# Kernel tuning notes

Measured on AMD Instinct MI355X. Metric: run time of the kernel, lower is better.

## Reference

```python
import jax, jax.numpy as jnp
import numpy as np

N_NODES = 50000
N_EDGES = 1600000
N_FEAT = 128
DIM = 128
N_GRAPHS = 128
BN_EPS = 1e-5


def setup_inputs() -> dict:
    key = jax.random.key(0)
    ks = jax.random.split(key, 16)
    x = jax.random.normal(ks[0], (N_NODES, N_FEAT), dtype=jnp.float32)
    edge_index = jax.random.randint(ks[1], (2, N_EDGES), 0, N_NODES)
    batch = jnp.sort(jax.random.randint(ks[2], (N_NODES,), 0, N_GRAPHS))
    def lin(k, fin, fout):
        return jax.random.normal(k, (fin, fout), dtype=jnp.float32) / np.sqrt(fin).astype(np.float32)
    inp = {"x": x, "edge_index": edge_index, "batch": batch}
    fins = [N_FEAT, DIM, DIM]
    for i in range(3):
        inp[f"W{i}"] = lin(ks[3 + i], fins[i], DIM)
        inp[f"b{i}"] = jnp.zeros((DIM,), jnp.float32)
        inp[f"g{i}"] = jnp.ones((DIM,), jnp.float32)
        inp[f"be{i}"] = jnp.zeros((DIM,), jnp.float32)
    return inp


def _gcn_norm(edge_index, n):
    # add self loops, symmetric normalization D^-1/2 (A+I) D^-1/2
    loop = jnp.arange(n, dtype=edge_index.dtype)
    src = jnp.concatenate([edge_index[0], loop])
    dst = jnp.concatenate([edge_index[1], loop])
    deg = jax.ops.segment_sum(jnp.ones_like(src, dtype=jnp.float32), dst, num_segments=n)
    dinv = jnp.where(deg > 0, jax.lax.rsqrt(deg), 0.0)
    norm = dinv[src] * dinv[dst]  # [E+N]
    return src, dst, norm


def _gcn_conv(h, W, b, src, dst, norm, n):
    h = h @ W                      # [N, D]
    msg = h[src] * norm[:, None]   # [E+N, D] gather + scale
    agg = jax.ops.segment_sum(msg, dst, num_segments=n)
    return agg + b


def _batchnorm(h, g, be):
    mu = jnp.mean(h, axis=0)
    var = jnp.mean(jnp.square(h - mu), axis=0)  # biased, training-mode BN
    return (h - mu) * jax.lax.rsqrt(var + BN_EPS) * g + be


def reference(x, edge_index, batch, W0, b0, g0, be0, W1, b1, g1, be1, W2, b2, g2, be2):
    n = x.shape[0]
    src, dst, norm = _gcn_norm(edge_index, n)
    params = [(W0, b0, g0, be0), (W1, b1, g1, be1), (W2, b2, g2, be2)]
    h = x
    pools = []
    for (W, b, g, be) in params:
        h = jax.nn.relu(_gcn_conv(h, W, b, src, dst, norm, n))
        h = _batchnorm(h, g, be)
        pools.append(jax.ops.segment_sum(h, batch, num_segments=N_GRAPHS))
    return jnp.concatenate(pools, axis=1)  # [N_GRAPHS, 3*DIM]
```

## Files before the change

kernel.cpp:

```cpp
#include <hip/hip_runtime.h>
#include <hip/hip_bf16.h>

#define N_GRAPHS 128
#define BN_EPS 1e-5f
#define CHUNK 8192
#define NBU 512
#define CAP 8192

typedef short bf16x8 __attribute__((ext_vector_type(8)));
typedef short s16x4 __attribute__((ext_vector_type(4)));
typedef float f32x4 __attribute__((ext_vector_type(4)));

__device__ __forceinline__ unsigned short f2b(float f) {
    unsigned int u = __builtin_bit_cast(unsigned int, f);
    u += 0x7FFFu + ((u >> 16) & 1u);
    return (unsigned short)(u >> 16);
}
__device__ __forceinline__ float b2f_lo(unsigned int p) {
    return __builtin_bit_cast(float, p << 16);
}
__device__ __forceinline__ float b2f_hi(unsigned int p) {
    return __builtin_bit_cast(float, p & 0xFFFF0000u);
}

__global__ __launch_bounds__(512) void bin_chunks(const int* __restrict__ src,
                                                  const int* __restrict__ dst,
                                                  unsigned int* __restrict__ bpairs,
                                                  int* __restrict__ cnts,
                                                  int* __restrict__ cbase, int E) {
    __shared__ int lhist[NBU], lscan[NBU], lfill[NBU];
    int tid = threadIdx.x;
    int c0 = blockIdx.x * CHUNK;
    int ecnt = min(CHUNK, E - c0);
    lhist[tid] = 0;
    __syncthreads();
    for (int i = tid; i < ecnt; i += 512)
        atomicAdd(&lhist[((unsigned)dst[c0 + i]) >> 7], 1);
    __syncthreads();
    int orig = lhist[tid];
    lscan[tid] = orig;
    __syncthreads();
    for (int off = 1; off < NBU; off <<= 1) {
        int t = (tid >= off) ? lscan[tid - off] : 0;
        __syncthreads();
        lscan[tid] += t;
        __syncthreads();
    }
    int excl = lscan[tid] - orig;
    cnts[blockIdx.x * NBU + tid] = orig;
    cbase[blockIdx.x * NBU + tid] = excl;
    lfill[tid] = 0;
    __syncthreads();
    lscan[tid] = excl;
    __syncthreads();
    for (int i = tid; i < ecnt; i += 512) {
        int d = dst[c0 + i], s = src[c0 + i];
        int b = ((unsigned)d) >> 7;
        int pos = lscan[b] + atomicAdd(&lfill[b], 1);
        bpairs[c0 + pos] = ((unsigned)(d & 127) << 25) | (unsigned)s;
    }
}

__global__ __launch_bounds__(512) void bucket_scan(const int* __restrict__ cnts,
                                                   int* __restrict__ bucket_base, int nchunks) {
    __shared__ int s[NBU];
    int b = threadIdx.x;
    int tot = 0;
    for (int c = 0; c < nchunks; ++c) tot += cnts[c * NBU + b];
    s[b] = tot;
    __syncthreads();
    for (int off = 1; off < NBU; off <<= 1) {
        int t = (b >= off) ? s[b - off] : 0;
        __syncthreads();
        s[b] += t;
        __syncthreads();
    }
    bucket_base[b] = s[b] - tot;
}

__global__ __launch_bounds__(256) void bucket_csr(const unsigned int* __restrict__ bpairs,
                                                  const int* __restrict__ cnts,
                                                  const int* __restrict__ cbase,
                                                  const int* __restrict__ bucket_base,
                                                  int* __restrict__ rowp,
                                                  int* __restrict__ degarr,
                                                  float* __restrict__ dinv,
                                                  int* __restrict__ csr,
                                                  int nchunks, int N) {
    __shared__ unsigned int lpr[CAP];
    __shared__ int lcsr[CAP];
    __shared__ int ccnt[256], cofs[256], cb[256];
    __shared__ int lhist[128], lofs[128], lfill[128];
    int tid = threadIdx.x;
    int b = blockIdx.x;
    int bb = bucket_base[b];
    int total = bucket_base[b + 1] - bb;
    if (total > CAP) total = CAP;

    ccnt[tid] = (tid < nchunks) ? cnts[tid * NBU + b] : 0;
    cb[tid]   = (tid < nchunks) ? cbase[tid * NBU + b] : 0;
    cofs[tid] = ccnt[tid];
    __syncthreads();
    int orig = cofs[tid];
    for (int off = 1; off < 256; off <<= 1) {
        int t = (tid >= off) ? cofs[tid - off] : 0;
        __syncthreads();
        cofs[tid] += t;
        __syncthreads();
    }
    int o = cofs[tid] - orig;
    if (tid < nchunks) {
        int len = ccnt[tid];
        const unsigned int* p = bpairs + (size_t)tid * CHUNK + cb[tid];
        for (int i = 0; i < len; ++i) {
            int q = o + i;
            if (q < CAP) lpr[q] = p[i];
        }
    }
    if (tid < 128) { lhist[tid] = 0; lfill[tid] = 0; }
    __syncthreads();
    for (int i = tid; i < total; i += 256)
        atomicAdd(&lhist[lpr[i] >> 25], 1);
    __syncthreads();
    if (tid < 128) lofs[tid] = lhist[tid];
    __syncthreads();
    for (int off = 1; off < 128; off <<= 1) {
        int t = 0;
        if (tid < 128 && tid >= off) t = lofs[tid - off];
        __syncthreads();
        if (tid < 128) lofs[tid] += t;
        __syncthreads();
    }
    if (tid < 128) {
        int v = b * 128 + tid;
        if (v < N) {
            int dg = lhist[tid];
            degarr[v] = dg;
            rowp[v] = bb + lofs[tid] - dg;
            dinv[v] = rsqrtf((float)(dg + 1));
        }
    }
    __syncthreads();
    for (int i = tid; i < total; i += 256) {
        unsigned int pr = lpr[i];
        int dl = pr >> 25;
        int pos = lofs[dl] - lhist[dl] + atomicAdd(&lfill[dl], 1);
        if (pos < CAP) lcsr[pos] = (int)(pr & 0x1FFFFFFu);
    }
    __syncthreads();
    for (int i = tid; i < total; i += 256) csr[bb + i] = lcsr[i];
}

template <int AF32>
__global__ __launch_bounds__(256) void gemm_mfma(const void* __restrict__ Avoid,
                                                 const float* __restrict__ W,
                                                 unsigned short* __restrict__ Cb, int N) {
    __shared__ unsigned short sWt[128 * 128];
    int tid = threadIdx.x;
    for (int i = tid; i < 128 * 128; i += 256) {
        int k = i >> 7, c = i & 127;
        int kk = k & 31, k0 = k >> 5;
        int hi = (kk >> 2) & 3;
        int e = (kk & 3) + 4 * (kk >> 4);
        int idx = c * 128 + k0 * 32 + hi * 8 + e;
        sWt[idx ^ ((c & 7) << 3)] = f2b(W[i]);
    }
    __syncthreads();

    int wave = tid >> 6, lane = tid & 63;
    int lo4 = lane & 15, hi = lane >> 4;
    int rowBase = blockIdx.x * 256 + wave * 64;

    f32x4 acc[8][4];
#pragma unroll
    for (int ct = 0; ct < 8; ++ct)
#pragma unroll
        for (int rt = 0; rt < 4; ++rt) acc[ct][rt] = (f32x4){0.f, 0.f, 0.f, 0.f};

    const float* Af = (const float*)Avoid;
    const unsigned short* Ab = (const unsigned short*)Avoid;

    for (int k0 = 0; k0 < 128; k0 += 32) {
        bf16x8 bfrag[4];
#pragma unroll
        for (int rt = 0; rt < 4; ++rt) {
            int r = rowBase + rt * 16 + lo4;
            if (r >= N) r = N - 1;
            if (AF32) {
                float4 f0 = *(const float4*)(Af + (size_t)r * 128 + k0 + 4 * hi);
                float4 f1 = *(const float4*)(Af + (size_t)r * 128 + k0 + 16 + 4 * hi);
                bf16x8 f;
                f[0] = (short)f2b(f0.x); f[1] = (short)f2b(f0.y);
                f[2] = (short)f2b(f0.z); f[3] = (short)f2b(f0.w);
                f[4] = (short)f2b(f1.x); f[5] = (short)f2b(f1.y);
                f[6] = (short)f2b(f1.z); f[7] = (short)f2b(f1.w);
                bfrag[rt] = f;
            } else {
                s16x4 a0 = *(const s16x4*)(Ab + (size_t)r * 128 + k0 + 4 * hi);
                s16x4 a1 = *(const s16x4*)(Ab + (size_t)r * 128 + k0 + 16 + 4 * hi);
                bf16x8 f;
                f[0] = a0[0]; f[1] = a0[1]; f[2] = a0[2]; f[3] = a0[3];
                f[4] = a1[0]; f[5] = a1[1]; f[6] = a1[2]; f[7] = a1[3];
                bfrag[rt] = f;
            }
        }
        int kq = k0 >> 5;
#pragma unroll
        for (int ct = 0; ct < 8; ++ct) {
            int c = ct * 16 + lo4;
            int idx = (c * 128 + kq * 32 + hi * 8) ^ ((c & 7) << 3);
            bf16x8 af = *(const bf16x8*)(sWt + idx);
#pragma unroll
            for (int rt = 0; rt < 4; ++rt)
                acc[ct][rt] = __builtin_amdgcn_mfma_f32_16x16x32_bf16(af, bfrag[rt], acc[ct][rt], 0, 0, 0);
        }
    }

#pragma unroll
    for (int rt = 0; rt < 4; ++rt) {
        int r = rowBase + rt * 16 + lo4;
        if (r < N) {
#pragma unroll
            for (int ct = 0; ct < 8; ++ct) {
                int c0 = ct * 16 + hi * 4;
                ushort4 s;
                s.x = f2b(acc[ct][rt][0]);
                s.y = f2b(acc[ct][rt][1]);
                s.z = f2b(acc[ct][rt][2]);
                s.w = f2b(acc[ct][rt][3]);
                *(ushort4*)(Cb + (size_t)r * 128 + c0) = s;
            }
        }
    }
}

__global__ __launch_bounds__(256) void agg_relu_b16(const unsigned int* __restrict__ hW32,
                                                    const int* __restrict__ rowp,
                                                    const int* __restrict__ cnt,
                                                    const int* __restrict__ csr,
                                                    const float* __restrict__ dinv,
                                                    const float* __restrict__ bias,
                                                    unsigned int* __restrict__ z32, int N) {
    int wave = threadIdx.x >> 6, lane = threadIdx.x & 63;
    int v = blockIdx.x * 4 + wave;
    if (v >= N) return;
    int beg = rowp[v];
    int num = cnt[v];
    float s0 = 0.f, s1 = 0.f;
    int i = 0;
    for (; i + 4 <= num; i += 4) {
        int u0 = csr[beg + i + 0];
        int u1 = csr[beg + i + 1];
        int u2 = csr[beg + i + 2];
        int u3 = csr[beg + i + 3];
        float w0 = dinv[u0], w1 = dinv[u1], w2 = dinv[u2], w3 = dinv[u3];
        unsigned int p0 = hW32[(size_t)u0 * 64 + lane];
        unsigned int p1 = hW32[(size_t)u1 * 64 + lane];
        unsigned int p2 = hW32[(size_t)u2 * 64 + lane];
        unsigned int p3 = hW32[(size_t)u3 * 64 + lane];
        s0 += w0 * b2f_lo(p0) + w1 * b2f_lo(p1) + w2 * b2f_lo(p2) + w3 * b2f_lo(p3);
        s1 += w0 * b2f_hi(p0) + w1 * b2f_hi(p1) + w2 * b2f_hi(p2) + w3 * b2f_hi(p3);
    }
    for (; i < num; ++i) {
        int u = csr[beg + i];
        float w = dinv[u];
        unsigned int p = hW32[(size_t)u * 64 + lane];
        s0 += w * b2f_lo(p);
        s1 += w * b2f_hi(p);
    }
    float dv = dinv[v];
    unsigned int pv = hW32[(size_t)v * 64 + lane];
    s0 = dv * s0 + dv * dv * b2f_lo(pv) + bias[2 * lane];
    s1 = dv * s1 + dv * dv * b2f_hi(pv) + bias[2 * lane + 1];
    unsigned int po = (unsigned int)f2b(fmaxf(s0, 0.f)) | ((unsigned int)f2b(fmaxf(s1, 0.f)) << 16);
    z32[(size_t)v * 64 + lane] = po;
}

__global__ __launch_bounds__(256) void bn_stats_b16(const unsigned int* __restrict__ z32,
                                                    float* __restrict__ stats, int N) {
    int lane = threadIdx.x & 63, sub = threadIdx.x >> 6;
    float s0 = 0.f, s1 = 0.f, q0 = 0.f, q1 = 0.f;
    for (int v = blockIdx.x * 4 + sub; v < N; v += gridDim.x * 4) {
        unsigned int p = z32[(size_t)v * 64 + lane];
        float a = b2f_lo(p), c = b2f_hi(p);
        s0 += a; q0 = fmaf(a, a, q0);
        s1 += c; q1 = fmaf(c, c, q1);
    }
    __shared__ float ls[256][4];
    ls[threadIdx.x][0] = s0; ls[threadIdx.x][1] = s1;
    ls[threadIdx.x][2] = q0; ls[threadIdx.x][3] = q1;
    __syncthreads();
    if (sub == 0) {
        for (int k = 1; k < 4; ++k) {
            s0 += ls[lane + 64 * k][0]; s1 += ls[lane + 64 * k][1];
            q0 += ls[lane + 64 * k][2]; q1 += ls[lane + 64 * k][3];
        }
        atomicAdd(&stats[2 * lane], s0);
        atomicAdd(&stats[2 * lane + 1], s1);
        atomicAdd(&stats[128 + 2 * lane], q0);
        atomicAdd(&stats[129 + 2 * lane], q1);
    }
}

__global__ void bn_finalize(const float* __restrict__ stats, const float* __restrict__ g,
                            const float* __restrict__ be, float* __restrict__ ss, float invN) {
    int d = threadIdx.x;
    float mu = stats[d] * invN;
    float var = stats[128 + d] * invN - mu * mu;
    float sc = g[d] * rsqrtf(var + BN_EPS);
    ss[d] = sc;
    ss[128 + d] = be[d] - mu * sc;
}

__global__ __launch_bounds__(64) void apply_pool_b16(const unsigned int* __restrict__ z32,
                                                     const float* __restrict__ ss,
                                                     const int* __restrict__ batch,
                                                     float* __restrict__ out,
                                                     unsigned int* __restrict__ zb,
                                                     int layer, int N) {
    __shared__ int gb[32];
    int lane = threadIdx.x;
    int v0 = blockIdx.x * 32;
    int vend = min(v0 + 32, N);
    int cntv = vend - v0;
    if (lane < cntv) gb[lane] = batch[v0 + lane];
    __syncthreads();
    float sc0 = ss[2 * lane], sc1 = ss[2 * lane + 1];
    float sh0 = ss[128 + 2 * lane], sh1 = ss[129 + 2 * lane];
    float a0 = 0.f, a1 = 0.f;
    int cur = gb[0];
    for (int j = 0; j < cntv; ++j) {
        unsigned int p = z32[(size_t)(v0 + j) * 64 + lane];
        float x0 = fmaf(b2f_lo(p), sc0, sh0);
        float x1 = fmaf(b2f_hi(p), sc1, sh1);
        if (zb) zb[(size_t)(v0 + j) * 64 + lane] =
            (unsigned int)f2b(x0) | ((unsigned int)f2b(x1) << 16);
        int g = gb[j];
        if (g != cur) {
            atomicAdd(&out[(size_t)cur * 384 + layer * 128 + 2 * lane], a0);
            atomicAdd(&out[(size_t)cur * 384 + layer * 128 + 2 * lane + 1], a1);
            a0 = a1 = 0.f;
            cur = g;
        }
        a0 += x0; a1 += x1;
    }
    atomicAdd(&out[(size_t)cur * 384 + layer * 128 + 2 * lane], a0);
    atomicAdd(&out[(size_t)cur * 384 + layer * 128 + 2 * lane + 1], a1);
}

extern "C" void kernel_launch(void* const* d_in, const int* in_sizes, int n_in,
                              void* d_out, int out_size, void* d_ws, size_t ws_size,
                              hipStream_t stream) {
    const float* x    = (const float*)d_in[0];
    const int* eidx   = (const int*)d_in[1];
    const int* batch  = (const int*)d_in[2];

    const int N = in_sizes[2];
    const int E = in_sizes[1] / 2;
    const int* src = eidx;
    const int* dst = eidx + E;

    const int nchunks = (E + CHUNK - 1) / CHUNK;
    const int NB = (N + 127) / 128;

    size_t off = 0;
    auto alloc = [&](size_t bytes) {
        void* p = (char*)d_ws + off;
        off += (bytes + 255) & ~(size_t)255;
        return p;
    };
    unsigned short* hWb = (unsigned short*)alloc((size_t)N * 128 * 2);
    unsigned int* zb    = (unsigned int*)alloc((size_t)N * 64 * 4);
    unsigned int* z32   = (unsigned int*)alloc((size_t)N * 64 * 4);
    unsigned int* bpairs= (unsigned int*)alloc((size_t)nchunks * CHUNK * 4);
    int*   csr   = (int*)alloc((size_t)E * 4);
    int*   cnts  = (int*)alloc((size_t)nchunks * NBU * 4);
    int*   cbase = (int*)alloc((size_t)nchunks * NBU * 4);
    int*   bbase = (int*)alloc((size_t)(NBU + 1) * 4);
    int*   degar = (int*)alloc((size_t)N * 4);
    int*   rowp  = (int*)alloc((size_t)N * 4);
    float* dinv  = (float*)alloc((size_t)N * 4);
    float* stats = (float*)alloc(3 * 256 * 4);
    float* ss    = (float*)alloc(3 * 256 * 4);

    float* out = (float*)d_out;

    hipMemsetAsync(stats, 0, 3 * 256 * 4, stream);
    hipMemsetAsync(out, 0, (size_t)N_GRAPHS * 384 * 4, stream);

    bin_chunks<<<nchunks, 512, 0, stream>>>(src, dst, bpairs, cnts, cbase, E);
    bucket_scan<<<1, 512, 0, stream>>>(cnts, bbase, nchunks);
    bucket_csr<<<NB, 256, 0, stream>>>(bpairs, cnts, cbase, bbase, rowp, degar, dinv, csr,
                                       nchunks, N);

    const int gemm_blocks = (N + 255) / 256;
    const int agg_blocks  = (N + 3) / 4;
    const int pool_blocks = (N + 31) / 32;

    for (int l = 0; l < 3; ++l) {
        const float* W  = (const float*)d_in[3 + 4 * l];
        const float* b  = (const float*)d_in[4 + 4 * l];
        const float* g  = (const float*)d_in[5 + 4 * l];
        const float* be = (const float*)d_in[6 + 4 * l];

        if (l == 0)
            gemm_mfma<1><<<gemm_blocks, 256, 0, stream>>>((const void*)x, W, hWb, N);
        else
            gemm_mfma<0><<<gemm_blocks, 256, 0, stream>>>((const void*)zb, W, hWb, N);

        agg_relu_b16<<<agg_blocks, 256, 0, stream>>>((const unsigned int*)hWb, rowp, degar, csr,
                                                     dinv, b, z32, N);
        bn_stats_b16<<<256, 256, 0, stream>>>(z32, stats + l * 256, N);
        bn_finalize<<<1, 128, 0, stream>>>(stats + l * 256, g, be, ss + l * 256, 1.0f / N);
        apply_pool_b16<<<pool_blocks, 64, 0, stream>>>(z32, ss + l * 256, batch, out,
                                                       (l < 2) ? zb : (unsigned int*)nullptr, l, N);
    }
}
```

Baseline: 525.2 us.

## Fold BN affine into next GEMM, slab-partition features for aggregation, atomic bucket totals

Folds the BatchNorm scale into the next layer's weights and the shift into a per-column bias computed in bn_finalize. This removes the normalized zb write in apply_pool, and the next GEMM reads z32 directly. The GEMM output becomes a 4-slab layout of 32 columns each, and aggregation runs one slab per block, with 4 lanes-groups over 16 dwords splitting neighbors and reducing by shuffles, so the gather working set per slab is smaller and more cache-friendly. Bucket totals are accumulated atomically in bin_chunks instead of serially summed in bucket_scan. The cost is 4x more aggregation blocks re-reading the CSR and dinv per slab, and bf16 rounding of the scaled weights.

```diff
diff --git a/kernel.cpp b/kernel.cpp
--- a/kernel.cpp
+++ b/kernel.cpp
@@ -27,7 +27,8 @@
                                                   const int* __restrict__ dst,
                                                   unsigned int* __restrict__ bpairs,
                                                   int* __restrict__ cnts,
-                                                  int* __restrict__ cbase, int E) {
+                                                  int* __restrict__ cbase,
+                                                  int* __restrict__ btot, int E) {
     __shared__ int lhist[NBU], lscan[NBU], lfill[NBU];
     int tid = threadIdx.x;
     int c0 = blockIdx.x * CHUNK;
@@ -38,6 +39,7 @@
         atomicAdd(&lhist[((unsigned)dst[c0 + i]) >> 7], 1);
     __syncthreads();
     int orig = lhist[tid];
+    atomicAdd(&btot[tid], orig);
     lscan[tid] = orig;
     __syncthreads();
     for (int off = 1; off < NBU; off <<= 1) {
@@ -61,12 +63,11 @@
     }
 }
 
-__global__ __launch_bounds__(512) void bucket_scan(const int* __restrict__ cnts,
-                                                   int* __restrict__ bucket_base, int nchunks) {
+__global__ __launch_bounds__(512) void bucket_scan(const int* __restrict__ btot,
+                                                   int* __restrict__ bucket_base) {
     __shared__ int s[NBU];
     int b = threadIdx.x;
-    int tot = 0;
-    for (int c = 0; c < nchunks; ++c) tot += cnts[c * NBU + b];
+    int tot = btot[b];
     s[b] = tot;
     __syncthreads();
     for (int off = 1; off < NBU; off <<= 1) {
@@ -154,16 +155,20 @@
 template <int AF32>
 __global__ __launch_bounds__(256) void gemm_mfma(const void* __restrict__ Avoid,
                                                  const float* __restrict__ W,
+                                                 const float* __restrict__ ssPrev,
+                                                 const float* __restrict__ wb,
                                                  unsigned short* __restrict__ Cb, int N) {
     __shared__ unsigned short sWt[128 * 128];
     int tid = threadIdx.x;
     for (int i = tid; i < 128 * 128; i += 256) {
         int k = i >> 7, c = i & 127;
+        float w = W[i];
+        if (!AF32) w *= ssPrev[k];
         int kk = k & 31, k0 = k >> 5;
         int hi = (kk >> 2) & 3;
         int e = (kk & 3) + 4 * (kk >> 4);
         int idx = c * 128 + k0 * 32 + hi * 8 + e;
-        sWt[idx ^ ((c & 7) << 3)] = f2b(W[i]);
+        sWt[idx ^ ((c & 7) << 3)] = f2b(w);
     }
     __syncthreads();
 
@@ -223,57 +228,62 @@
 #pragma unroll
             for (int ct = 0; ct < 8; ++ct) {
                 int c0 = ct * 16 + hi * 4;
+                float4 wbv = make_float4(0.f, 0.f, 0.f, 0.f);
+                if (!AF32) wbv = *(const float4*)(wb + c0);
                 ushort4 s;
-                s.x = f2b(acc[ct][rt][0]);
-                s.y = f2b(acc[ct][rt][1]);
-                s.z = f2b(acc[ct][rt][2]);
-                s.w = f2b(acc[ct][rt][3]);
-                *(ushort4*)(Cb + (size_t)r * 128 + c0) = s;
+                s.x = f2b(acc[ct][rt][0] + wbv.x);
+                s.y = f2b(acc[ct][rt][1] + wbv.y);
+                s.z = f2b(acc[ct][rt][2] + wbv.z);
+                s.w = f2b(acc[ct][rt][3] + wbv.w);
+                int q = c0 >> 5;
+                *(ushort4*)(Cb + (size_t)q * N * 32 + (size_t)r * 32 + (c0 & 31)) = s;
             }
         }
     }
 }
 
-__global__ __launch_bounds__(256) void agg_relu_b16(const unsigned int* __restrict__ hW32,
-                                                    const int* __restrict__ rowp,
-                                                    const int* __restrict__ cnt,
-                                                    const int* __restrict__ csr,
-                                                    const float* __restrict__ dinv,
-                                                    const float* __restrict__ bias,
-                                                    unsigned int* __restrict__ z32, int N) {
+__global__ __launch_bounds__(256) void agg_relu_slab(const unsigned int* __restrict__ hW32,
+                                                     const int* __restrict__ rowp,
+                                                     const int* __restrict__ cnt,
+                                                     const int* __restrict__ csr,
+                                                     const float* __restrict__ dinv,
+                                                     const float* __restrict__ bias,
+                                                     unsigned int* __restrict__ z32,
+                                                     int ngroups, int N) {
+    int q = blockIdx.x / ngroups;
+    int group = blockIdx.x % ngroups;
     int wave = threadIdx.x >> 6, lane = threadIdx.x & 63;
-    int v = blockIdx.x * 4 + wave;
+    int v = group * 4 + wave;
     if (v >= N) return;
+    int dd = lane & 15, e = lane >> 4;
+    const unsigned int* hWq = hW32 + (size_t)q * N * 16;
+
     int beg = rowp[v];
     int num = cnt[v];
     float s0 = 0.f, s1 = 0.f;
-    int i = 0;
-    for (; i + 4 <= num; i += 4) {
-        int u0 = csr[beg + i + 0];
-        int u1 = csr[beg + i + 1];
-        int u2 = csr[beg + i + 2];
-        int u3 = csr[beg + i + 3];
-        float w0 = dinv[u0], w1 = dinv[u1], w2 = dinv[u2], w3 = dinv[u3];
-        unsigned int p0 = hW32[(size_t)u0 * 64 + lane];
-        unsigned int p1 = hW32[(size_t)u1 * 64 + lane];
-        unsigned int p2 = hW32[(size_t)u2 * 64 + lane];
-        unsigned int p3 = hW32[(size_t)u3 * 64 + lane];
-        s0 += w0 * b2f_lo(p0) + w1 * b2f_lo(p1) + w2 * b2f_lo(p2) + w3 * b2f_lo(p3);
-        s1 += w0 * b2f_hi(p0) + w1 * b2f_hi(p1) + w2 * b2f_hi(p2) + w3 * b2f_hi(p3);
-    }
-    for (; i < num; ++i) {
-        int u = csr[beg + i];
-        float w = dinv[u];
-        unsigned int p = hW32[(size_t)u * 64 + lane];
+    int iters = (num + 3) >> 2;
+    for (int i = 0; i < iters; ++i) {
+        int idx = 4 * i + e;
+        bool ok = idx < num;
+        int u = ok ? csr[beg + idx] : v;
+        float w = ok ? dinv[u] : 0.f;
+        unsigned int p = hWq[(size_t)u * 16 + dd];
         s0 += w * b2f_lo(p);
         s1 += w * b2f_hi(p);
     }
-    float dv = dinv[v];
-    unsigned int pv = hW32[(size_t)v * 64 + lane];
-    s0 = dv * s0 + dv * dv * b2f_lo(pv) + bias[2 * lane];
-    s1 = dv * s1 + dv * dv * b2f_hi(pv) + bias[2 * lane + 1];
-    unsigned int po = (unsigned int)f2b(fmaxf(s0, 0.f)) | ((unsigned int)f2b(fmaxf(s1, 0.f)) << 16);
-    z32[(size_t)v * 64 + lane] = po;
+    s0 += __shfl_xor(s0, 16, 64);
+    s0 += __shfl_xor(s0, 32, 64);
+    s1 += __shfl_xor(s1, 16, 64);
+    s1 += __shfl_xor(s1, 32, 64);
+    if (e == 0) {
+        float dv = dinv[v];
+        unsigned int pv = hWq[(size_t)v * 16 + dd];
+        float r0 = dv * s0 + dv * dv * b2f_lo(pv) + bias[q * 32 + 2 * dd];
+        float r1 = dv * s1 + dv * dv * b2f_hi(pv) + bias[q * 32 + 2 * dd + 1];
+        unsigned int po = (unsigned int)f2b(fmaxf(r0, 0.f)) |
+                          ((unsigned int)f2b(fmaxf(r1, 0.f)) << 16);
+        z32[(size_t)v * 64 + q * 16 + dd] = po;
+    }
 }
 
 __global__ __launch_bounds__(256) void bn_stats_b16(const unsigned int* __restrict__ z32,
@@ -302,21 +312,32 @@
     }
 }
 
-__global__ void bn_finalize(const float* __restrict__ stats, const float* __restrict__ g,
-                            const float* __restrict__ be, float* __restrict__ ss, float invN) {
+__global__ void bn_finalize_wb(const float* __restrict__ stats, const float* __restrict__ g,
+                               const float* __restrict__ be, float* __restrict__ ss,
+                               const float* __restrict__ Wnext, float* __restrict__ wb,
+                               float invN) {
+    __shared__ float shv[128];
     int d = threadIdx.x;
     float mu = stats[d] * invN;
     float var = stats[128 + d] * invN - mu * mu;
     float sc = g[d] * rsqrtf(var + BN_EPS);
+    float sh = be[d] - mu * sc;
     ss[d] = sc;
-    ss[128 + d] = be[d] - mu * sc;
+    ss[128 + d] = sh;
+    shv[d] = sh;
+    __syncthreads();
+    if (Wnext) {
+        float acc = 0.f;
+#pragma unroll 4
+        for (int k = 0; k < 128; ++k) acc = fmaf(shv[k], Wnext[k * 128 + d], acc);
+        wb[d] = acc;
+    }
 }
 
 __global__ __launch_bounds__(64) void apply_pool_b16(const unsigned int* __restrict__ z32,
                                                      const float* __restrict__ ss,
                                                      const int* __restrict__ batch,
                                                      float* __restrict__ out,
-                                                     unsigned int* __restrict__ zb,
                                                      int layer, int N) {
     __shared__ int gb[32];
     int lane = threadIdx.x;
@@ -333,8 +354,6 @@
         unsigned int p = z32[(size_t)(v0 + j) * 64 + lane];
         float x0 = fmaf(b2f_lo(p), sc0, sh0);
         float x1 = fmaf(b2f_hi(p), sc1, sh1);
-        if (zb) zb[(size_t)(v0 + j) * 64 + lane] =
-            (unsigned int)f2b(x0) | ((unsigned int)f2b(x1) << 16);
         int g = gb[j];
         if (g != cur) {
             atomicAdd(&out[(size_t)cur * 384 + layer * 128 + 2 * lane], a0);
@@ -370,31 +389,34 @@
         return p;
     };
     unsigned short* hWb = (unsigned short*)alloc((size_t)N * 128 * 2);
-    unsigned int* zb    = (unsigned int*)alloc((size_t)N * 64 * 4);
     unsigned int* z32   = (unsigned int*)alloc((size_t)N * 64 * 4);
     unsigned int* bpairs= (unsigned int*)alloc((size_t)nchunks * CHUNK * 4);
     int*   csr   = (int*)alloc((size_t)E * 4);
     int*   cnts  = (int*)alloc((size_t)nchunks * NBU * 4);
     int*   cbase = (int*)alloc((size_t)nchunks * NBU * 4);
     int*   bbase = (int*)alloc((size_t)(NBU + 1) * 4);
+    int*   btot  = (int*)alloc((size_t)NBU * 4);
     int*   degar = (int*)alloc((size_t)N * 4);
     int*   rowp  = (int*)alloc((size_t)N * 4);
     float* dinv  = (float*)alloc((size_t)N * 4);
     float* stats = (float*)alloc(3 * 256 * 4);
     float* ss    = (float*)alloc(3 * 256 * 4);
+    float* wbuf  = (float*)alloc(2 * 128 * 4);
 
     float* out = (float*)d_out;
 
     hipMemsetAsync(stats, 0, 3 * 256 * 4, stream);
+    hipMemsetAsync(btot, 0, (size_t)NBU * 4, stream);
     hipMemsetAsync(out, 0, (size_t)N_GRAPHS * 384 * 4, stream);
 
-    bin_chunks<<<nchunks, 512, 0, stream>>>(src, dst, bpairs, cnts, cbase, E);
-    bucket_scan<<<1, 512, 0, stream>>>(cnts, bbase, nchunks);
+    bin_chunks<<<nchunks, 512, 0, stream>>>(src, dst, bpairs, cnts, cbase, btot, E);
+    bucket_scan<<<1, 512, 0, stream>>>(btot, bbase);
     bucket_csr<<<NB, 256, 0, stream>>>(bpairs, cnts, cbase, bbase, rowp, degar, dinv, csr,
                                        nchunks, N);
 
     const int gemm_blocks = (N + 255) / 256;
-    const int agg_blocks  = (N + 3) / 4;
+    const int ngroups     = (N + 3) / 4;
+    const int agg_blocks  = 4 * ngroups;
     const int pool_blocks = (N + 31) / 32;
 
     for (int l = 0; l < 3; ++l) {
@@ -404,15 +426,20 @@
         const float* be = (const float*)d_in[6 + 4 * l];
 
         if (l == 0)
-            gemm_mfma<1><<<gemm_blocks, 256, 0, stream>>>((const void*)x, W, hWb, N);
+            gemm_mfma<1><<<gemm_blocks, 256, 0, stream>>>((const void*)x, W, nullptr, nullptr,
+                                                          hWb, N);
         else
-            gemm_mfma<0><<<gemm_blocks, 256, 0, stream>>>((const void*)zb, W, hWb, N);
-
-        agg_relu_b16<<<agg_blocks, 256, 0, stream>>>((const unsigned int*)hWb, rowp, degar, csr,
-                                                     dinv, b, z32, N);
+            gemm_mfma<0><<<gemm_blocks, 256, 0, stream>>>((const void*)z32, W,
+                                                          ss + (l - 1) * 256, wbuf + (l - 1) * 128,
+                                                          hWb, N);
+
+        agg_relu_slab<<<agg_blocks, 256, 0, stream>>>((const unsigned int*)hWb, rowp, degar, csr,
+                                                      dinv, b, z32, ngroups, N);
         bn_stats_b16<<<256, 256, 0, stream>>>(z32, stats + l * 256, N);
-        bn_finalize<<<1, 128, 0, stream>>>(stats + l * 256, g, be, ss + l * 256, 1.0f / N);
-        apply_pool_b16<<<pool_blocks, 64, 0, stream>>>(z32, ss + l * 256, batch, out,
-                                                       (l < 2) ? zb : (unsigned int*)nullptr, l, N);
-    }
-}
+        bn_finalize_wb<<<1, 128, 0, stream>>>(stats + l * 256, g, be, ss + l * 256,
+                                              (l < 2) ? (const float*)d_in[3 + 4 * (l + 1)]
+                                                      : (const float*)nullptr,
+                                              wbuf + l * 128, 1.0f / N);
+        apply_pool_b16<<<pool_blocks, 64, 0, stream>>>(z32, ss + l * 256, batch, out, l, N);
+    }
+}
```

Result: slower. 820.7 us (+56.3%).
